# Kernel tuning notes

Measured on AMD Instinct MI355X. Metric: run time of the kernel, lower is better.

Reference implementation:

```python
import jax, jax.numpy as jnp
import numpy as np

D_MODEL = 1024
N_HEADS = 16
D_K = D_MODEL // N_HEADS
B, L = 2, 2048


def setup_inputs() -> dict:
    key = jax.random.key(0)
    ks = jax.random.split(key, 11)
    s = 1.0 / np.sqrt(D_MODEL)
    return {
        "q": jax.random.normal(ks[0], (B, L, D_MODEL), jnp.float32),
        "k": jax.random.normal(ks[1], (B, L, D_MODEL), jnp.float32),
        "v": jax.random.normal(ks[2], (B, L, D_MODEL), jnp.float32),
        "w_q": jax.random.normal(ks[3], (D_MODEL, D_MODEL), jnp.float32) * s,
        "b_q": jnp.zeros((D_MODEL,), jnp.float32),
        "w_k": jax.random.normal(ks[4], (D_MODEL, D_MODEL), jnp.float32) * s,
        "b_k": jnp.zeros((D_MODEL,), jnp.float32),
        "w_v": jax.random.normal(ks[5], (D_MODEL, D_MODEL), jnp.float32) * s,
        "b_v": jnp.zeros((D_MODEL,), jnp.float32),
        "w_o": jax.random.normal(ks[6], (D_MODEL, D_MODEL), jnp.float32) * s,
        "b_o": jnp.zeros((D_MODEL,), jnp.float32),
    }


def reference(q, k, v, w_q, b_q, w_k, b_k, w_v, b_v, w_o, b_o):
    b, l, _ = q.shape
    # QKV projections (flax Linear: x @ W + b)
    query = q @ w_q + b_q
    key_ = k @ w_k + b_k
    value = v @ w_v + b_v
    # (B, L, D) -> (B, H, L, d_k)
    query = query.reshape(b, l, N_HEADS, D_K).transpose(0, 2, 1, 3)
    key_ = key_.reshape(b, l, N_HEADS, D_K).transpose(0, 2, 1, 3)
    value = value.reshape(b, l, N_HEADS, D_K).transpose(0, 2, 1, 3)
    # scaled dot-product attention; full (B, H, L, L) score matrix per original
    scores = jnp.einsum("bhqd,bhkd->bhqk", query, key_) / jnp.sqrt(
        jnp.asarray(D_K, query.dtype)
    )
    attn = jax.nn.softmax(scores, axis=-1)
    x = jnp.einsum("bhqk,bhkd->bhqd", attn, value)
    # (B, H, L, d_k) -> (B, L, D)
    x = x.transpose(0, 2, 1, 3).reshape(b, l, D_MODEL)
    return x @ w_o + b_o
```

## Files before the change

kernel.cpp:

```cpp
#include <hip/hip_runtime.h>
#include <hip/hip_bf16.h>


#define D_MODELC 1024
#define N_HEADSC 16
#define D_KC 64
#define BBC 2
#define LLC 2048
#define MMC (BBC * LLC)

typedef __attribute__((ext_vector_type(8))) short v8s;
typedef __attribute__((ext_vector_type(4))) float v4f;

__device__ __forceinline__ float bf2f(unsigned short u) {
    union { unsigned int i; float f; } x;
    x.i = ((unsigned int)u) << 16;
    return x.f;
}
__device__ __forceinline__ unsigned short f2bf(float f) {
    union { float f; unsigned int i; } x;
    x.f = f;
    unsigned int r = x.i + 0x7fffu + ((x.i >> 16) & 1u);
    return (unsigned short)(r >> 16);
}
__device__ __forceinline__ unsigned int pk2bf(float a, float b) {
    __hip_bfloat162 h = __float22bfloat162_rn(make_float2(a, b));
    return *(unsigned int*)&h;
}

#define AS1 __attribute__((address_space(1)))
#define AS3 __attribute__((address_space(3)))

__global__ __launch_bounds__(256) void wtrans(const float* __restrict__ w0,
                                              const float* __restrict__ w1,
                                              const float* __restrict__ w2,
                                              const float* __restrict__ w3,
                                              unsigned short* __restrict__ out) {
    __shared__ unsigned short T[64][65];
    const int z = blockIdx.z;
    const float* W = z == 0 ? w0 : (z == 1 ? w1 : (z == 2 ? w2 : w3));
    unsigned short* O = out + (size_t)z * D_MODELC * D_MODELC;
    const int k0 = blockIdx.y * 64, n0 = blockIdx.x * 64;
    const int c = threadIdx.x & 63, r4 = threadIdx.x >> 6;
#pragma unroll
    for (int i = 0; i < 16; i++) {
        int r = i * 4 + r4;
        T[r][c] = f2bf(W[(size_t)(k0 + r) * D_MODELC + n0 + c]);
    }
    __syncthreads();
#pragma unroll
    for (int i = 0; i < 16; i++) {
        int r = i * 4 + r4;
        O[(size_t)(n0 + r) * D_MODELC + k0 + c] = T[c][r];
    }
}

__global__ __launch_bounds__(256) void vtrans(const unsigned short* __restrict__ Vp,
                                              unsigned short* __restrict__ Vt) {
    __shared__ __align__(16) unsigned short T[64][68];
    const int bh = blockIdx.y;
    const int b = bh >> 4, h = bh & 15;
    const int j0 = blockIdx.x * 64;
    const int t = threadIdx.x;
#pragma unroll
    for (int i = 0; i < 2; i++) {
        int c = i * 256 + t;
        int row = c >> 3, ch = c & 7;
        *(v8s*)&T[row][ch * 8] =
            *(const v8s*)&Vp[((size_t)(b * LLC + j0 + row)) * D_MODELC + h * 64 + ch * 8];
    }
    __syncthreads();
#pragma unroll
    for (int i = 0; i < 2; i++) {
        int c = i * 256 + t;
        int drow = c >> 3, jch = c & 7;
        v8s pk;
#pragma unroll
        for (int u = 0; u < 8; u++) pk[u] = (short)T[jch * 8 + u][drow];
        *(v8s*)&Vt[((size_t)bh * 64 + drow) * LLC + j0 + jch * 8] = pk;
    }
}

template <int MT, int SEGS, bool A_F32, bool OUT_F32>
__global__ __launch_bounds__(256) void gemm_tile(
    const void* __restrict__ A0, const void* __restrict__ A1, const void* __restrict__ A2,
    const unsigned short* __restrict__ Wt,
    const float* __restrict__ bias0, const float* __restrict__ bias1,
    const float* __restrict__ bias2,
    void* __restrict__ C0, void* __restrict__ C1, void* __restrict__ C2,
    float scale0, float scale1, float scale2) {
    const int K = D_MODELC, N = D_MODELC;
    constexpr int MI = MT / 32;
    constexpr int MB = MMC / MT;
    constexpr int PER = SEGS * MB / 8;
    __shared__ __align__(16) unsigned short As[MT * 64];
    __shared__ __align__(16) unsigned short Bs[128 * 64];

    const int t = threadIdx.x;
    const int w = t >> 6, lane = t & 63;
    const int quad = lane >> 4, m15 = lane & 15;
    const int wr = w >> 1, wc = w & 1;
    const int sw = m15 & 7;

    const int flat = blockIdx.x;
    const int xcd = flat & 7;
    const int slot0 = flat >> 3;
    const int group = xcd * PER + (slot0 >> 3);
    const int nb = slot0 & 7;
    const int seg = group / MB;
    const int mb = group % MB;
    const int n0 = nb * 128;
    const int m0 = mb * MT;

    const void* Ap = seg == 0 ? A0 : (seg == 1 ? A1 : A2);
    const unsigned short* Wp = Wt + (size_t)seg * D_MODELC * D_MODELC;
    const float* bias = seg == 0 ? bias0 : (seg == 1 ? bias1 : bias2);
    void* Cp = seg == 0 ? C0 : (seg == 1 ? C1 : C2);
    const float scl = seg == 0 ? scale0 : (seg == 1 ? scale1 : scale2);

    v4f acc[MI][4];
#pragma unroll
    for (int mi = 0; mi < MI; mi++)
#pragma unroll
        for (int ni = 0; ni < 4; ni++) acc[mi][ni] = (v4f){0.f, 0.f, 0.f, 0.f};

    for (int k0 = 0; k0 < K; k0 += 64) {
#pragma unroll
        for (int i = 0; i < 4; i++) {
            int c = i * 256 + t;
            int row = c >> 3, slot = c & 7;
            int j = slot ^ (row & 7);
            const unsigned short* g = Wp + (size_t)(n0 + row) * K + k0 + j * 8;
            __builtin_amdgcn_global_load_lds(
                (const AS1 unsigned int*)g,
                (AS3 unsigned int*)(Bs + (size_t)c * 8), 16, 0, 0);
        }
        if (A_F32) {
#pragma unroll
            for (int i = 0; i < MT / 32; i++) {
                int c = i * 256 + t;
                int row = c >> 3, slot = c & 7;
                int j = slot ^ (row & 7);
                const float* src = (const float*)Ap + (size_t)(m0 + row) * K + k0 + j * 8;
                float4 f0 = ((const float4*)src)[0];
                float4 f1 = ((const float4*)src)[1];
                uint4 pk;
                pk.x = pk2bf(f0.x, f0.y);
                pk.y = pk2bf(f0.z, f0.w);
                pk.z = pk2bf(f1.x, f1.y);
                pk.w = pk2bf(f1.z, f1.w);
                *(uint4*)&As[(size_t)c * 8] = pk;
            }
        } else {
#pragma unroll
            for (int i = 0; i < MT / 32; i++) {
                int c = i * 256 + t;
                int row = c >> 3, slot = c & 7;
                int j = slot ^ (row & 7);
                const unsigned short* g =
                    (const unsigned short*)Ap + (size_t)(m0 + row) * K + k0 + j * 8;
                __builtin_amdgcn_global_load_lds(
                    (const AS1 unsigned int*)g,
                    (AS3 unsigned int*)(As + (size_t)c * 8), 16, 0, 0);
            }
        }
        __syncthreads();

#pragma unroll
        for (int kk = 0; kk < 2; kk++) {
            v8s a[MI], bfr[4];
#pragma unroll
            for (int mi = 0; mi < MI; mi++)
                a[mi] = *(const v8s*)&As[(wr * (MT / 2) + mi * 16 + m15) * 64 +
                                         (((kk * 4 + quad) ^ sw) * 8)];
#pragma unroll
            for (int ni = 0; ni < 4; ni++)
                bfr[ni] = *(const v8s*)&Bs[(wc * 64 + ni * 16 + m15) * 64 +
                                           (((kk * 4 + quad) ^ sw) * 8)];
#pragma unroll
            for (int mi = 0; mi < MI; mi++)
#pragma unroll
                for (int ni = 0; ni < 4; ni++)
                    acc[mi][ni] = __builtin_amdgcn_mfma_f32_16x16x32_bf16(
                        a[mi], bfr[ni], acc[mi][ni], 0, 0, 0);
        }
        __syncthreads();
    }

#pragma unroll
    for (int ni = 0; ni < 4; ni++) {
        int col = n0 + wc * 64 + ni * 16 + m15;
        float bv = bias[col];
#pragma unroll
        for (int mi = 0; mi < MI; mi++) {
#pragma unroll
            for (int r = 0; r < 4; r++) {
                int row = m0 + wr * (MT / 2) + mi * 16 + quad * 4 + r;
                float v = (acc[mi][ni][r] + bv) * scl;
                if (OUT_F32)
                    ((float*)Cp)[(size_t)row * N + col] = v;
                else
                    ((unsigned short*)Cp)[(size_t)row * N + col] = f2bf(v);
            }
        }
    }
}

__global__ __launch_bounds__(256) void attn_mfma(const unsigned short* __restrict__ Qp,
                                                 const unsigned short* __restrict__ Kp,
                                                 const unsigned short* __restrict__ Vt,
                                                 unsigned short* __restrict__ X) {
    __shared__ __align__(16) unsigned short lds[8192 + 8192 + 128 * 72];
    unsigned short* Kb = lds;
    unsigned short* Vb = lds + 8192;
    unsigned short* PQ = lds + 16384;

    const int t = threadIdx.x;
    const int w = t >> 6, lane = t & 63;
    const int quad = lane >> 4, m15 = lane & 15;
    const int bh = blockIdx.y;
    const int b = bh >> 4, h = bh & 15;
    const int q0 = blockIdx.x * 128;
    const size_t hd = (size_t)h * 64;
    const int sw = m15 & 7;

#pragma unroll
    for (int i = 0; i < 4; i++) {
        int chunk = i * 256 + t;
        int row = chunk >> 3, slot = chunk & 7;
        int j = slot ^ (row & 7);
        const unsigned short* g =
            Qp + ((size_t)(b * LLC + q0 + row)) * D_MODELC + hd + j * 8;
        __builtin_amdgcn_global_load_lds((const AS1 unsigned int*)g,
                                         (AS3 unsigned int*)(PQ + (i * 256 + w * 64) * 8),
                                         16, 0, 0);
    }
    {
#pragma unroll
        for (int i = 0; i < 2; i++) {
            int chunk = i * 256 + t;
            int row = chunk >> 3, slot = chunk & 7;
            int j = slot ^ (row & 7);
            int gr = 4 * (row & 15) + (row >> 4);
            const unsigned short* g =
                Kp + ((size_t)(b * LLC + 0 + gr)) * D_MODELC + hd + j * 8;
            __builtin_amdgcn_global_load_lds((const AS1 unsigned int*)g,
                                             (AS3 unsigned int*)(Kb + (i * 256 + w * 64) * 8),
                                             16, 0, 0);
        }
#pragma unroll
        for (int i = 0; i < 2; i++) {
            int chunk = i * 256 + t;
            int row = chunk >> 3, slot = chunk & 7;
            int j = slot ^ (row & 7);
            const unsigned short* g = Vt + ((size_t)(bh * 64 + row)) * LLC + 0 + j * 8;
            __builtin_amdgcn_global_load_lds((const AS1 unsigned int*)g,
                                             (AS3 unsigned int*)(Vb + (i * 256 + w * 64) * 8),
                                             16, 0, 0);
        }
    }
    __syncthreads();

    v8s qa[2][2];
#pragma unroll
    for (int mi = 0; mi < 2; mi++)
#pragma unroll
        for (int kk = 0; kk < 2; kk++)
            qa[mi][kk] = *(const v8s*)&PQ[(w * 32 + mi * 16 + m15) * 64 +
                                          (((kk * 4 + quad) ^ sw) * 8)];
    __syncthreads();

    v8s ones;
#pragma unroll
    for (int u = 0; u < 8; u++) ones[u] = (short)0x3F80;

    v4f O[2][4];
#pragma unroll
    for (int mi = 0; mi < 2; mi++)
#pragma unroll
        for (int db = 0; db < 4; db++) O[mi][db] = (v4f){0.f, 0.f, 0.f, 0.f};
    v4f lacc[2] = {(v4f){0.f, 0.f, 0.f, 0.f}, (v4f){0.f, 0.f, 0.f, 0.f}};

    for (int it = 0; it < 32; it++) {
        const int cur = it & 1;
        unsigned short* Kc = Kb + cur * 4096;
        unsigned short* Vc = Vb + cur * 4096;
        if (it < 31) {
            unsigned short* Kn = Kb + (cur ^ 1) * 4096;
            unsigned short* Vn = Vb + (cur ^ 1) * 4096;
            const int k0n = (it + 1) * 64;
#pragma unroll
            for (int i = 0; i < 2; i++) {
                int chunk = i * 256 + t;
                int row = chunk >> 3, slot = chunk & 7;
                int j = slot ^ (row & 7);
                int gr = 4 * (row & 15) + (row >> 4);
                const unsigned short* g =
                    Kp + ((size_t)(b * LLC + k0n + gr)) * D_MODELC + hd + j * 8;
                __builtin_amdgcn_global_load_lds(
                    (const AS1 unsigned int*)g,
                    (AS3 unsigned int*)(Kn + (i * 256 + w * 64) * 8), 16, 0, 0);
            }
#pragma unroll
            for (int i = 0; i < 2; i++) {
                int chunk = i * 256 + t;
                int row = chunk >> 3, slot = chunk & 7;
                int j = slot ^ (row & 7);
                const unsigned short* g =
                    Vt + ((size_t)(bh * 64 + row)) * LLC + k0n + j * 8;
                __builtin_amdgcn_global_load_lds(
                    (const AS1 unsigned int*)g,
                    (AS3 unsigned int*)(Vn + (i * 256 + w * 64) * 8), 16, 0, 0);
            }
        }

        v4f S[2][4];
#pragma unroll
        for (int mi = 0; mi < 2; mi++)
#pragma unroll
            for (int ns = 0; ns < 4; ns++) S[mi][ns] = (v4f){0.f, 0.f, 0.f, 0.f};
#pragma unroll
        for (int kk = 0; kk < 2; kk++) {
#pragma unroll
            for (int ns = 0; ns < 4; ns++) {
                v8s kf = *(const v8s*)&Kc[(ns * 16 + m15) * 64 +
                                          (((kk * 4 + quad) ^ sw) * 8)];
#pragma unroll
                for (int mi = 0; mi < 2; mi++)
                    S[mi][ns] =
                        __builtin_amdgcn_mfma_f32_16x16x32_bf16(qa[mi][kk], kf, S[mi][ns], 0, 0, 0);
            }
        }

#pragma unroll
        for (int mi = 0; mi < 2; mi++) {
#pragma unroll
            for (int r = 0; r < 4; r++) {
                int prow = w * 32 + mi * 16 + quad * 4 + r;
                float e0 = __builtin_amdgcn_exp2f(S[mi][0][r]);
                float e1 = __builtin_amdgcn_exp2f(S[mi][1][r]);
                float e2 = __builtin_amdgcn_exp2f(S[mi][2][r]);
                float e3 = __builtin_amdgcn_exp2f(S[mi][3][r]);
                uint2 pk;
                pk.x = pk2bf(e0, e1);
                pk.y = pk2bf(e2, e3);
                *(uint2*)&PQ[prow * 72 + 4 * m15] = pk;
            }
        }

#pragma unroll
        for (int kk = 0; kk < 2; kk++) {
            v8s a0 = *(const v8s*)&PQ[(w * 32 + 0 * 16 + m15) * 72 + kk * 32 + quad * 8];
            v8s a1 = *(const v8s*)&PQ[(w * 32 + 1 * 16 + m15) * 72 + kk * 32 + quad * 8];
            lacc[0] = __builtin_amdgcn_mfma_f32_16x16x32_bf16(a0, ones, lacc[0], 0, 0, 0);
            lacc[1] = __builtin_amdgcn_mfma_f32_16x16x32_bf16(a1, ones, lacc[1], 0, 0, 0);
#pragma unroll
            for (int db = 0; db < 4; db++) {
                v8s vf = *(const v8s*)&Vc[(db * 16 + m15) * 64 +
                                          (((kk * 4 + quad) ^ sw) * 8)];
                O[0][db] = __builtin_amdgcn_mfma_f32_16x16x32_bf16(a0, vf, O[0][db], 0, 0, 0);
                O[1][db] = __builtin_amdgcn_mfma_f32_16x16x32_bf16(a1, vf, O[1][db], 0, 0, 0);
            }
        }
        __syncthreads();
    }

#pragma unroll
    for (int mi = 0; mi < 2; mi++) {
#pragma unroll
        for (int r = 0; r < 4; r++) {
            float inv = 1.f / lacc[mi][r];
            int row = q0 + w * 32 + mi * 16 + quad * 4 + r;
#pragma unroll
            for (int db = 0; db < 4; db++) {
                X[((size_t)(b * LLC + row)) * D_MODELC + hd + db * 16 + m15] =
                    f2bf(O[mi][db][r] * inv);
            }
        }
    }
}

extern "C" void kernel_launch(void* const* d_in, const int* in_sizes, int n_in,
                              void* d_out, int out_size, void* d_ws, size_t ws_size,
                              hipStream_t stream) {
    const float* q = (const float*)d_in[0];
    const float* k = (const float*)d_in[1];
    const float* v = (const float*)d_in[2];
    const float* w_q = (const float*)d_in[3];
    const float* b_q = (const float*)d_in[4];
    const float* w_k = (const float*)d_in[5];
    const float* b_k = (const float*)d_in[6];
    const float* w_v = (const float*)d_in[7];
    const float* b_v = (const float*)d_in[8];
    const float* w_o = (const float*)d_in[9];
    const float* b_o = (const float*)d_in[10];

    const size_t elems = (size_t)MMC * D_MODELC;
    unsigned short* Qp = (unsigned short*)d_ws;
    unsigned short* Kp = Qp + elems;
    unsigned short* Vp = Kp + elems;
    unsigned short* Wt = Vp + elems;
    unsigned short* X = Qp;
    unsigned short* Vt = (unsigned short*)d_out;

    const float QSCALE = 0.125f * 1.44269504088896340736f;

    wtrans<<<dim3(16, 16, 4), 256, 0, stream>>>(w_q, w_k, w_v, w_o, Wt);

    gemm_tile<128, 3, true, false><<<768, 256, 0, stream>>>(
        q, k, v, Wt, b_q, b_k, b_v, Qp, Kp, Vp, QSCALE, 1.f, 1.f);

    vtrans<<<dim3(LLC / 64, BBC * N_HEADSC), 256, 0, stream>>>(Vp, Vt);

    attn_mfma<<<dim3(LLC / 128, BBC * N_HEADSC), 256, 0, stream>>>(Qp, Kp, Vt, X);

    gemm_tile<64, 1, false, true><<<512, 256, 0, stream>>>(
        X, X, X, Wt + (size_t)3 * D_MODELC * D_MODELC, b_o, b_o, b_o,
        d_out, d_out, d_out, 1.f, 1.f, 1.f);
}
```

Baseline: 245.1 us.

## Double-buffer GEMM LDS tiles and prefetch next K-slice during MFMA

Converts the projection GEMM main loop into a software pipeline. Weight tiles (and bf16 A tiles) are double-buffered in LDS via async global_load_lds. For f32 A inputs, the next slice is held in registers and converted to bf16 after compute. This is meant to hide global load latency behind the MFMA work, at the cost of twice the LDS, more registers, and an extra barrier on the f32 path, which may reduce occupancy.

```diff
diff --git a/kernel.cpp b/kernel.cpp
--- a/kernel.cpp
+++ b/kernel.cpp
@@ -93,8 +93,9 @@
     constexpr int MI = MT / 32;
     constexpr int MB = MMC / MT;
     constexpr int PER = SEGS * MB / 8;
-    __shared__ __align__(16) unsigned short As[MT * 64];
-    __shared__ __align__(16) unsigned short Bs[128 * 64];
+    constexpr int ABUF = A_F32 ? 1 : 2;
+    __shared__ __align__(16) unsigned short As[ABUF][MT * 64];
+    __shared__ __align__(16) unsigned short Bs[2][128 * 64];
 
     const int t = threadIdx.x;
     const int w = t >> 6, lane = t & 63;
@@ -118,13 +119,9 @@
     void* Cp = seg == 0 ? C0 : (seg == 1 ? C1 : C2);
     const float scl = seg == 0 ? scale0 : (seg == 1 ? scale1 : scale2);
 
-    v4f acc[MI][4];
-#pragma unroll
-    for (int mi = 0; mi < MI; mi++)
-#pragma unroll
-        for (int ni = 0; ni < 4; ni++) acc[mi][ni] = (v4f){0.f, 0.f, 0.f, 0.f};
-
-    for (int k0 = 0; k0 < K; k0 += 64) {
+    float4 af[MI][2];
+
+    auto stageB = [&](int buf, int k0) {
 #pragma unroll
         for (int i = 0; i < 4; i++) {
             int c = i * 256 + t;
@@ -133,49 +130,83 @@
             const unsigned short* g = Wp + (size_t)(n0 + row) * K + k0 + j * 8;
             __builtin_amdgcn_global_load_lds(
                 (const AS1 unsigned int*)g,
-                (AS3 unsigned int*)(Bs + (size_t)c * 8), 16, 0, 0);
-        }
-        if (A_F32) {
-#pragma unroll
-            for (int i = 0; i < MT / 32; i++) {
-                int c = i * 256 + t;
-                int row = c >> 3, slot = c & 7;
-                int j = slot ^ (row & 7);
-                const float* src = (const float*)Ap + (size_t)(m0 + row) * K + k0 + j * 8;
-                float4 f0 = ((const float4*)src)[0];
-                float4 f1 = ((const float4*)src)[1];
-                uint4 pk;
-                pk.x = pk2bf(f0.x, f0.y);
-                pk.y = pk2bf(f0.z, f0.w);
-                pk.z = pk2bf(f1.x, f1.y);
-                pk.w = pk2bf(f1.z, f1.w);
-                *(uint4*)&As[(size_t)c * 8] = pk;
-            }
-        } else {
-#pragma unroll
-            for (int i = 0; i < MT / 32; i++) {
-                int c = i * 256 + t;
-                int row = c >> 3, slot = c & 7;
-                int j = slot ^ (row & 7);
-                const unsigned short* g =
-                    (const unsigned short*)Ap + (size_t)(m0 + row) * K + k0 + j * 8;
-                __builtin_amdgcn_global_load_lds(
-                    (const AS1 unsigned int*)g,
-                    (AS3 unsigned int*)(As + (size_t)c * 8), 16, 0, 0);
-            }
-        }
-        __syncthreads();
-
+                (AS3 unsigned int*)(&Bs[buf][0] + (size_t)c * 8), 16, 0, 0);
+        }
+    };
+    auto stageA_lds = [&](int buf, int k0) {
+#pragma unroll
+        for (int i = 0; i < MI; i++) {
+            int c = i * 256 + t;
+            int row = c >> 3, slot = c & 7;
+            int j = slot ^ (row & 7);
+            const unsigned short* g =
+                (const unsigned short*)Ap + (size_t)(m0 + row) * K + k0 + j * 8;
+            __builtin_amdgcn_global_load_lds(
+                (const AS1 unsigned int*)g,
+                (AS3 unsigned int*)(&As[buf][0] + (size_t)c * 8), 16, 0, 0);
+        }
+    };
+    auto loadA = [&](int k0) {
+#pragma unroll
+        for (int i = 0; i < MI; i++) {
+            int c = i * 256 + t;
+            int row = c >> 3, slot = c & 7;
+            int j = slot ^ (row & 7);
+            const float* src = (const float*)Ap + (size_t)(m0 + row) * K + k0 + j * 8;
+            af[i][0] = ((const float4*)src)[0];
+            af[i][1] = ((const float4*)src)[1];
+        }
+    };
+    auto writeA = [&]() {
+#pragma unroll
+        for (int i = 0; i < MI; i++) {
+            int c = i * 256 + t;
+            uint4 pk;
+            pk.x = pk2bf(af[i][0].x, af[i][0].y);
+            pk.y = pk2bf(af[i][0].z, af[i][0].w);
+            pk.z = pk2bf(af[i][1].x, af[i][1].y);
+            pk.w = pk2bf(af[i][1].z, af[i][1].w);
+            *(uint4*)&As[0][(size_t)c * 8] = pk;
+        }
+    };
+
+    v4f acc[MI][4];
+#pragma unroll
+    for (int mi = 0; mi < MI; mi++)
+#pragma unroll
+        for (int ni = 0; ni < 4; ni++) acc[mi][ni] = (v4f){0.f, 0.f, 0.f, 0.f};
+
+    if constexpr (A_F32) {
+        loadA(0);
+        writeA();
+    } else {
+        stageA_lds(0, 0);
+    }
+    stageB(0, 0);
+    __syncthreads();
+
+    int cur = 0;
+    for (int k0 = 0; k0 < K; k0 += 64) {
+        const bool pf = (k0 + 64) < K;
+        const int nxt = cur ^ 1;
+        if (pf) {
+            if constexpr (A_F32) loadA(k0 + 64);
+            else stageA_lds(nxt, k0 + 64);
+            stageB(nxt, k0 + 64);
+        }
+
+        const unsigned short* Ac = A_F32 ? &As[0][0] : &As[cur][0];
+        const unsigned short* Bc = &Bs[cur][0];
 #pragma unroll
         for (int kk = 0; kk < 2; kk++) {
             v8s a[MI], bfr[4];
 #pragma unroll
             for (int mi = 0; mi < MI; mi++)
-                a[mi] = *(const v8s*)&As[(wr * (MT / 2) + mi * 16 + m15) * 64 +
+                a[mi] = *(const v8s*)&Ac[(wr * (MT / 2) + mi * 16 + m15) * 64 +
                                          (((kk * 4 + quad) ^ sw) * 8)];
 #pragma unroll
             for (int ni = 0; ni < 4; ni++)
-                bfr[ni] = *(const v8s*)&Bs[(wc * 64 + ni * 16 + m15) * 64 +
+                bfr[ni] = *(const v8s*)&Bc[(wc * 64 + ni * 16 + m15) * 64 +
                                            (((kk * 4 + quad) ^ sw) * 8)];
 #pragma unroll
             for (int mi = 0; mi < MI; mi++)
@@ -184,7 +215,13 @@
                     acc[mi][ni] = __builtin_amdgcn_mfma_f32_16x16x32_bf16(
                         a[mi], bfr[ni], acc[mi][ni], 0, 0, 0);
         }
+
+        if constexpr (A_F32) {
+            __syncthreads();
+            if (pf) writeA();
+        }
         __syncthreads();
+        cur = nxt;
     }
 
 #pragma unroll
```

Result: slower. 256.2 us (+4.5%).
